# Kernel tuning notes

Hardware: AMD Instinct MI355X
Metric: run time of the kernel (lower is better)

## Reference

```python
import jax, jax.numpy as jnp
import numpy as np

B, N, E, D, N_NODE = 512, 64, 64, 256, 200000
NEG = -9e15
ALPHA = 0.2  # leaky-relu slope from HGNN_ATT(..., 0.2, ...)


def _hgat_layer(x, adj_mask, w2, w3, a, a2, wc, w=None):
    """HyperGraphAttentionLayerSparse (HyperGAT), dense-masked vectorized form.
    x: [B,N,d_in], adj_mask: [B,E,N] bool. Returns (node [B,N,d], edge [B,E,d]).
    Eval mode: dropout is identity. concat=False so no ELU on output."""
    d = w2.shape[1]
    x4 = x @ w2                                            # [B,N,d]
    if w is not None:                                      # transfer=True path
        x = x @ w
    # node->edge attention: score = leakyrelu([word_context; x4_node] @ a), independent of edge idx
    s1 = jax.nn.leaky_relu(jnp.dot(wc, a[:d, 0]) + x4 @ a[d:, 0], ALPHA)   # [B,N]
    att_edge = jax.nn.softmax(jnp.where(adj_mask, s1[:, None, :], NEG), axis=2)  # [B,E,N]
    edge = att_edge @ x                                    # [B,E,d]
    edge4 = edge @ w3                                      # [B,E,d]
    # edge->node attention: score = leakyrelu([x4_node; edge4_edge] @ a2)
    s_pair = jax.nn.leaky_relu((x4 @ a2[:d, 0])[:, None, :] + (edge4 @ a2[d:, 0])[:, :, None], ALPHA)  # [B,E,N]
    att_node = jax.nn.softmax(jnp.swapaxes(jnp.where(adj_mask, s_pair, NEG), 1, 2), axis=2)  # [B,N,E]
    node = att_node @ edge                                 # [B,N,d]
    return node, edge


def setup_inputs() -> dict:
    key = jax.random.key(0)
    ks = jax.random.split(key, 16)
    stdv = 1.0 / np.sqrt(D)  # SessionGraph.reset_parameters uniform(-stdv, stdv)
    u = lambda k, shape: jax.random.uniform(k, shape, jnp.float32, -stdv, stdv)
    return {
        "inputs": jax.random.randint(ks[0], (B, N), 0, N_NODE, dtype=jnp.int32),
        "HT": (jax.random.uniform(ks[1], (B, E, N)) < 0.3).astype(jnp.int32),
        "G": jnp.zeros((1,), jnp.float32),
        "EG": jnp.zeros((1,), jnp.float32),
        "emb_w": u(ks[2], (N_NODE, D)),
        "emb2_w": u(ks[3], (N_NODE, D)),
        "g1_w2": u(ks[4], (D, D)),
        "g1_w3": u(ks[5], (D, D)),
        "g1_a": u(ks[6], (2 * D, 1)),
        "g1_a2": u(ks[7], (2 * D, 1)),
        "g1_wc": u(ks[8], (D,)),
        "g2_w": u(ks[9], (D, D)),
        "g2_w2": u(ks[10], (D, D)),
        "g2_w3": u(ks[11], (D, D)),
        "g2_a": u(ks[12], (2 * D, 1)),
        "g2_a2": u(ks[13], (2 * D, 1)),
        "g2_wc": u(ks[14], (D,)),
    }


def reference(inputs, HT, G, EG, emb_w, emb2_w, g1_w2, g1_w3, g1_a, g1_a2, g1_wc,
              g2_w, g2_w2, g2_w3, g2_a, g2_a2, g2_wc):
    adj_mask = HT > 0
    x = emb_w[inputs]                                      # [B,N,D] embedding gather
    residual = x
    # HGNN_ATT with step=2: gat1 (transfer=False) + residual, gat2 (transfer=True) + residual
    x, _ = _hgat_layer(x, adj_mask, g1_w2, g1_w3, g1_a, g1_a2, g1_wc)
    x = x + residual
    x, _ = _hgat_layer(x, adj_mask, g2_w2, g2_w3, g2_a, g2_a2, g2_wc, g2_w)
    x = x + residual
    nodes2 = emb2_w[inputs]                                # second embedding gather
    return (x, x, nodes2)  # (nodes, hidden, nodes2); hidden aliases nodes in the original
```

## Files before the change

### kernel.cpp

```cpp
#include <hip/hip_runtime.h>

#define BB 512
#define NN 64
#define EE 64
#define DD 256
#define BND (BB * NN * DD)
#define SA 68

typedef __attribute__((ext_vector_type(8))) short s8v;
typedef __attribute__((ext_vector_type(4))) float f4v;
typedef __attribute__((ext_vector_type(8))) unsigned short u16x8;

__device__ __forceinline__ unsigned short f2bf(float f) {
    unsigned int x = __float_as_uint(f);
    x = x + 0x7fffu + ((x >> 16) & 1u);
    return (unsigned short)(x >> 16);
}
__device__ __forceinline__ float bf2f(unsigned short u) {
    return __uint_as_float(((unsigned int)u) << 16);
}
__device__ __forceinline__ float lrelu(float v) { return v > 0.f ? v : 0.2f * v; }

#define WS_PREP  0
#define WS_P3B   8192
#define WS_WFRAG 12288

__global__ void prep_dots(const float* __restrict__ w2a, const float* __restrict__ w3a,
                          const float* __restrict__ aa, const float* __restrict__ a2a,
                          const float* __restrict__ wca,
                          const float* __restrict__ w2b, const float* __restrict__ w3b,
                          const float* __restrict__ ab, const float* __restrict__ a2b,
                          const float* __restrict__ wcb,
                          float* __restrict__ prep, float* __restrict__ p3b_ws) {
    const int t = threadIdx.x;
    const int blk = blockIdx.x;
    const int layer = blk >> 3;
    const int r0 = (blk & 7) * 32;
    __shared__ float vhi[256], v2lo[256], v2hi[256], red[256];
    const float* w2 = layer ? w2b : w2a;
    const float* w3 = layer ? w3b : w3a;
    const float* av = layer ? ab : aa;
    const float* a2 = layer ? a2b : a2a;
    vhi[t] = av[256 + t];
    v2lo[t] = a2[t];
    v2hi[t] = a2[256 + t];
    __syncthreads();
    const int row = r0 + (t >> 3), q = t & 7;
    const float* w2r = w2 + (size_t)row * DD + q * 32;
    const float* w3r = w3 + (size_t)row * DD + q * 32;
    float s1 = 0.f, s2 = 0.f, s3 = 0.f;
    #pragma unroll
    for (int c = 0; c < 8; c++) {
        float4 v = *(const float4*)&w2r[c * 4];
        float4 u = *(const float4*)&w3r[c * 4];
        float4 p1 = *(const float4*)&vhi[q * 32 + c * 4];
        float4 p2 = *(const float4*)&v2lo[q * 32 + c * 4];
        float4 p3 = *(const float4*)&v2hi[q * 32 + c * 4];
        s1 = fmaf(v.x, p1.x, fmaf(v.y, p1.y, fmaf(v.z, p1.z, fmaf(v.w, p1.w, s1))));
        s2 = fmaf(v.x, p2.x, fmaf(v.y, p2.y, fmaf(v.z, p2.z, fmaf(v.w, p2.w, s2))));
        s3 = fmaf(u.x, p3.x, fmaf(u.y, p3.y, fmaf(u.z, p3.z, fmaf(u.w, p3.w, s3))));
    }
    s1 += __shfl_xor(s1, 1); s1 += __shfl_xor(s1, 2); s1 += __shfl_xor(s1, 4);
    s2 += __shfl_xor(s2, 1); s2 += __shfl_xor(s2, 2); s2 += __shfl_xor(s2, 4);
    s3 += __shfl_xor(s3, 1); s3 += __shfl_xor(s3, 2); s3 += __shfl_xor(s3, 4);
    if (q == 0) {
        if (layer == 0) { prep[row] = s1; prep[256 + row] = s2; prep[512 + row] = s3; }
        else { prep[1024 + row] = s1; prep[1280 + row] = s2; p3b_ws[row] = s3; }
    }
    if ((blk & 7) == 0) {
        red[t] = layer ? (wcb[t] * ab[t]) : (wca[t] * aa[t]);
        __syncthreads();
        for (int o = 128; o > 0; o >>= 1) { if (t < o) red[t] += red[t + o]; __syncthreads(); }
        if (t == 0) prep[layer ? 1792 : 768] = red[0];
    }
}

__global__ void prep2_pack(const float* __restrict__ wtr, const float* __restrict__ p3b_ws,
                           float* __restrict__ prep, unsigned short* __restrict__ wfrag) {
    const int t = threadIdx.x, blk = blockIdx.x;
    __shared__ float p3[256];
    if (blk < 8) {
        p3[t] = p3b_ws[t];
        __syncthreads();
        const int row = blk * 32 + (t >> 3), q = t & 7;
        const float* wr = wtr + (size_t)row * DD + q * 32;
        float s = 0.f;
        #pragma unroll
        for (int c = 0; c < 8; c++) {
            float4 v = *(const float4*)&wr[c * 4];
            float4 p = *(const float4*)&p3[q * 32 + c * 4];
            s = fmaf(v.x, p.x, fmaf(v.y, p.y, fmaf(v.z, p.z, fmaf(v.w, p.w, s))));
        }
        s += __shfl_xor(s, 1); s += __shfl_xor(s, 2); s += __shfl_xor(s, 4);
        if (q == 0) prep[1536 + row] = s;
    } else {
        int gid = (blk - 8) * 256 + t;
        int l = gid & 63, frag = gid >> 6;
        int kc = frag >> 4, nt = frag & 15;
        int kb = kc * 32 + (l >> 4) * 8;
        int n = nt * 16 + (l & 15);
        u16x8 u;
        #pragma unroll
        for (int j = 0; j < 8; j++) u[j] = f2bf(wtr[(size_t)(kb + j) * DD + n]);
        *(u16x8*)(wfrag + (size_t)gid * 8) = u;
    }
}

__launch_bounds__(512, 4)
__global__ void mega(const int* __restrict__ inputs, const int* __restrict__ HT,
                     const float* __restrict__ emb_w, const float* __restrict__ emb2_w,
                     const float* __restrict__ prep, const unsigned short* __restrict__ wfrag,
                     float* __restrict__ out) {
    __shared__ unsigned short bufA[256 * SA];
    __shared__ unsigned short RA[64 * SA];
    __shared__ unsigned short RB[64 * SA];
    __shared__ unsigned short RC[64 * SA];
    __shared__ unsigned short RD[64 * SA];
    __shared__ unsigned short XT[16 * SA];
    __shared__ unsigned short pvs[6 * 256];
    __shared__ float dvs[384];
    __shared__ float db2[192];
    __shared__ float u1f[64], invdef[64];
    __shared__ unsigned long long mE[64], mN[64];

    const int b = blockIdx.x;
    const int t = threadIdx.x;
    const int lane = t & 63;
    const int w8 = t >> 6;
    const int l15 = lane & 15, lh = lane >> 4;

    for (int i = t; i < 1536; i += 512) {
        int off = i + (((i >> 8) >= 3) ? 256 : 0);
        pvs[i] = f2bf(prep[off]);
    }
    for (int i = t; i < 16 * SA; i += 512) XT[i] = 0;
    {
        const int rw = t >> 3, q8 = t & 7;
        const int idx = inputs[b * 64 + rw];
        const float* src = emb_w + (size_t)idx * DD + q8 * 32;
        #pragma unroll
        for (int c = 0; c < 8; c++) {
            float4 v = ((const float4*)src)[c];
            ushort4 u;
            u.x = f2bf(v.x); u.y = f2bf(v.y); u.z = f2bf(v.z); u.w = f2bf(v.w);
            *(ushort4*)&bufA[rw * 264 + q8 * 32 + c * 4] = u;
        }
    }
    float4 n2r[8];
    #pragma unroll
    for (int c = 0; c < 8; c++) {
        int i = t + 512 * c;
        int n = i >> 6, cc = i & 63;
        int idx = inputs[b * 64 + n];
        n2r[c] = ((const float4*)(emb2_w + (size_t)idx * DD))[cc];
    }
    #pragma unroll
    for (int i = 0; i < 8; i++) {
        int e = w8 * 8 + i;
        int hx = HT[((size_t)b * EE + e) * NN + lane];
        unsigned long long m = __ballot(hx > 0);
        if (lane == 0) mE[e] = m;
    }
    __syncthreads();

    if (w8 < 4) {
        const int wtile = w8 * 16;
        const int j = (l15 < 6) ? l15 : 5;
        f4v acc = {0.f, 0.f, 0.f, 0.f};
        #pragma unroll
        for (int kc = 0; kc < 8; kc++) {
            s8v a = *(const s8v*)&bufA[(wtile + l15) * 264 + kc * 32 + lh * 8];
            s8v bv = *(const s8v*)&pvs[j * 256 + kc * 32 + lh * 8];
            acc = __builtin_amdgcn_mfma_f32_16x16x32_bf16(a, bv, acc, 0, 0, 0);
        }
        if (l15 < 6) {
            #pragma unroll
            for (int rg = 0; rg < 4; rg++)
                dvs[l15 * 64 + wtile + lh * 4 + rg] = acc[rg];
        }
    } else if (w8 == 4) {
        unsigned long long acc = 0ull;
        for (int e = 0; e < 64; e++) acc |= ((mE[e] >> lane) & 1ull) << e;
        mN[lane] = acc;
    }
    __syncthreads();

    const int wr = (w8 & 3) * 16;
    const int wc = (w8 >> 2) * 32;
    const int row0 = wr + lh * 4;

    {
        float s1l = lrelu(prep[768] + dvs[lane]);
        float g1 = s1l;
        #pragma unroll
        for (int o = 32; o > 0; o >>= 1) g1 = fmaxf(g1, __shfl_xor(g1, o));
        float E1 = __expf(s1l - g1);
        #pragma unroll
        for (int i = 0; i < 8; i++) {
            int e = w8 * 8 + i;
            unsigned long long me = mE[e];
            float pe = (me == 0ull) ? 1.f : (((me >> lane) & 1ull) ? E1 : 0.f);
            unsigned short bf = f2bf(pe);
            RA[lane * SA + e] = bf;
            RC[e * SA + lane] = bf;
        }
    }
    __syncthreads();

    if (w8 < 4) {
        const int etile = w8 * 16;
        f4v acc = {0.f, 0.f, 0.f, 0.f};
        #pragma unroll
        for (int kc = 0; kc < 2; kc++) {
            u16x8 au;
            #pragma unroll
            for (int jj = 0; jj < 8; jj++) {
                int k = kc * 32 + lh * 8 + jj;
                float v = (l15 == 0) ? 1.f : ((l15 <= 4) ? dvs[(l15 + 1) * 64 + k] : 0.f);
                au[jj] = f2bf(v);
            }
            s8v bv = *(const s8v*)&RC[(etile + l15) * SA + kc * 32 + lh * 8];
            acc = __builtin_amdgcn_mfma_f32_16x16x32_bf16((s8v)au, bv, acc, 0, 0, 0);
        }
        int e = etile + l15;
        if (lh == 0) {
            float De = acc[0], We = acc[1];
            invdef[e] = 1.f / De;
            u1f[e] = We / De;
            XT[e] = f2bf(De);
            XT[1 * SA + e] = f2bf(acc[2]);
            XT[2 * SA + e] = f2bf(acc[3]);
        } else if (lh == 1) {
            XT[3 * SA + e] = f2bf(acc[0]);
        }
    }
    __syncthreads();

    {
        float t2l = dvs[64 + lane];
        float gt2 = t2l;
        #pragma unroll
        for (int o = 32; o > 0; o >>= 1) gt2 = fmaxf(gt2, __shfl_xor(gt2, o));
        float um = u1f[lane];
        #pragma unroll
        for (int o = 32; o > 0; o >>= 1) um = fmaxf(um, __shfl_xor(um, o));
        float M1 = lrelu(gt2 + um);
        float ul = u1f[lane];
        float ide = invdef[lane];
        #pragma unroll
        for (int i = 0; i < 8; i++) {
            int n = w8 * 8 + i;
            unsigned long long mn = mN[n];
            float t2n = dvs[64 + n];
            float pr = (mn == 0ull) ? 1.f
                     : (((mn >> lane) & 1ull) ? __expf(lrelu(t2n + ul) - M1) : 0.f);
            RB[n * SA + lane] = f2bf(pr * ide);
        }
    }
    __syncthreads();

    {
        f4v a0 = {0.f,0.f,0.f,0.f}, a1 = {0.f,0.f,0.f,0.f}, ax = {0.f,0.f,0.f,0.f};
        #pragma unroll
        for (int kc = 0; kc < 2; kc++) {
            s8v a  = *(const s8v*)&RB[(wr + l15) * SA + kc * 32 + lh * 8];
            s8v b0 = *(const s8v*)&RA[(wc + l15) * SA + kc * 32 + lh * 8];
            s8v b1 = *(const s8v*)&RA[(wc + 16 + l15) * SA + kc * 32 + lh * 8];
            s8v bx = *(const s8v*)&XT[l15 * SA + kc * 32 + lh * 8];
            a0 = __builtin_amdgcn_mfma_f32_16x16x32_bf16(a, b0, a0, 0, 0, 0);
            a1 = __builtin_amdgcn_mfma_f32_16x16x32_bf16(a, b1, a1, 0, 0, 0);
            ax = __builtin_amdgcn_mfma_f32_16x16x32_bf16(a, bx, ax, 0, 0, 0);
        }
        float invdn[4];
        #pragma unroll
        for (int rg = 0; rg < 4; rg++) invdn[rg] = 1.f / __shfl(ax[rg], lh << 4);
        int col0 = wc + l15, col1 = wc + 16 + l15;
        ushort4 u0, u1;
        #pragma unroll
        for (int rg = 0; rg < 4; rg++) {
            ((unsigned short*)&u0)[rg] = f2bf(a0[rg] * invdn[rg] + ((row0 + rg) == col0 ? 1.f : 0.f));
            ((unsigned short*)&u1)[rg] = f2bf(a1[rg] * invdn[rg] + ((row0 + rg) == col1 ? 1.f : 0.f));
        }
        *(ushort4*)&RD[col0 * SA + row0] = u0;
        *(ushort4*)&RD[col1 * SA + row0] = u1;
        if (w8 < 4 && l15 >= 1 && l15 <= 3) {
            int jj = l15 - 1;
            #pragma unroll
            for (int rg = 0; rg < 4; rg++)
                db2[jj * 64 + row0 + rg] = ax[rg] * invdn[rg] + dvs[(jj + 3) * 64 + row0 + rg];
        }
    }
    __syncthreads();

    {
        float s2l = lrelu(prep[1792] + db2[lane]);
        float g2 = s2l;
        #pragma unroll
        for (int o = 32; o > 0; o >>= 1) g2 = fmaxf(g2, __shfl_xor(g2, o));
        float E2 = __expf(s2l - g2);
        #pragma unroll
        for (int i = 0; i < 8; i++) {
            int e = w8 * 8 + i;
            unsigned long long me = mE[e];
            float pe = (me == 0ull) ? 1.f : (((me >> lane) & 1ull) ? E2 : 0.f);
            unsigned short bf = f2bf(pe);
            RA[lane * SA + e] = bf;
            RC[e * SA + lane] = bf;
        }
    }
    __syncthreads();

    if (w8 < 4) {
        const int etile = w8 * 16;
        f4v acc = {0.f, 0.f, 0.f, 0.f};
        #pragma unroll
        for (int kc = 0; kc < 2; kc++) {
            u16x8 au;
            #pragma unroll
            for (int jj = 0; jj < 8; jj++) {
                int k = kc * 32 + lh * 8 + jj;
                float v = (l15 == 0) ? 1.f : ((l15 == 1) ? db2[128 + k] : 0.f);
                au[jj] = f2bf(v);
            }
            s8v bv = *(const s8v*)&RC[(etile + l15) * SA + kc * 32 + lh * 8];
            acc = __builtin_amdgcn_mfma_f32_16x16x32_bf16((s8v)au, bv, acc, 0, 0, 0);
        }
        if (lh == 0) {
            int e = etile + l15;
            float De = acc[0], We = acc[1];
            invdef[e] = 1.f / De;
            u1f[e] = We / De;
            XT[e] = f2bf(De);
        }
    }
    __syncthreads();

    {
        float d1l = db2[64 + lane];
        float gd1 = d1l;
        #pragma unroll
        for (int o = 32; o > 0; o >>= 1) gd1 = fmaxf(gd1, __shfl_xor(gd1, o));
        float um = u1f[lane];
        #pragma unroll
        for (int o = 32; o > 0; o >>= 1) um = fmaxf(um, __shfl_xor(um, o));
        float M2 = lrelu(gd1 + um);
        float ul = u1f[lane];
        float ide = invdef[lane];
        #pragma unroll
        for (int i = 0; i < 8; i++) {
            int n = w8 * 8 + i;
            unsigned long long mn = mN[n];
            float d1n = db2[64 + n];
            float pr = (mn == 0ull) ? 1.f
                     : (((mn >> lane) & 1ull) ? __expf(lrelu(d1n + ul) - M2) : 0.f);
            RB[n * SA + lane] = f2bf(pr * ide);
        }
    }
    __syncthreads();

    {
        f4v a0 = {0.f,0.f,0.f,0.f}, a1 = {0.f,0.f,0.f,0.f}, ax = {0.f,0.f,0.f,0.f};
        #pragma unroll
        for (int kc = 0; kc < 2; kc++) {
            s8v a  = *(const s8v*)&RB[(wr + l15) * SA + kc * 32 + lh * 8];
            s8v b0 = *(const s8v*)&RA[(wc + l15) * SA + kc * 32 + lh * 8];
            s8v b1 = *(const s8v*)&RA[(wc + 16 + l15) * SA + kc * 32 + lh * 8];
            s8v bx = *(const s8v*)&XT[l15 * SA + kc * 32 + lh * 8];
            a0 = __builtin_amdgcn_mfma_f32_16x16x32_bf16(a, b0, a0, 0, 0, 0);
            a1 = __builtin_amdgcn_mfma_f32_16x16x32_bf16(a, b1, a1, 0, 0, 0);
            ax = __builtin_amdgcn_mfma_f32_16x16x32_bf16(a, bx, ax, 0, 0, 0);
        }
        float invdn[4];
        #pragma unroll
        for (int rg = 0; rg < 4; rg++) invdn[rg] = 1.f / __shfl(ax[rg], lh << 4);
        #pragma unroll
        for (int rg = 0; rg < 4; rg++) {
            RC[(row0 + rg) * SA + wc + l15] = f2bf(a0[rg] * invdn[rg]);
            RC[(row0 + rg) * SA + wc + 16 + l15] = f2bf(a1[rg] * invdn[rg]);
        }
    }
    __syncthreads();

    {
        f4v a0 = {0.f,0.f,0.f,0.f}, a1 = {0.f,0.f,0.f,0.f};
        #pragma unroll
        for (int kc = 0; kc < 2; kc++) {
            s8v a  = *(const s8v*)&RC[(wr + l15) * SA + kc * 32 + lh * 8];
            s8v b0 = *(const s8v*)&RD[(wc + l15) * SA + kc * 32 + lh * 8];
            s8v b1 = *(const s8v*)&RD[(wc + 16 + l15) * SA + kc * 32 + lh * 8];
            a0 = __builtin_amdgcn_mfma_f32_16x16x32_bf16(a, b0, a0, 0, 0, 0);
            a1 = __builtin_amdgcn_mfma_f32_16x16x32_bf16(a, b1, a1, 0, 0, 0);
        }
        #pragma unroll
        for (int rg = 0; rg < 4; rg++) {
            RA[(row0 + rg) * SA + wc + l15] = f2bf(a0[rg]);
            RA[(row0 + rg) * SA + wc + 16 + l15] = f2bf(a1[rg]);
        }
    }
    #pragma unroll
    for (int c = 0; c < 8; c++) {
        int i = t + 512 * c;
        int n = i >> 6, cc = i & 63;
        ((float4*)(out + (size_t)2 * BND + (size_t)(b * 64 + n) * DD))[cc] = n2r[c];
    }
    __syncthreads();

    const int cb8 = (w8 >> 2) * 8;
    unsigned short rres[8][4];
    {
        f4v acc[8];
        #pragma unroll
        for (int nt = 0; nt < 8; nt++) acc[nt] = (f4v){0.f, 0.f, 0.f, 0.f};
        const s8v* wf = (const s8v*)wfrag;
        #pragma unroll
        for (int kc = 0; kc < 8; kc++) {
            s8v a = *(const s8v*)&bufA[(wr + l15) * 264 + kc * 32 + lh * 8];
            #pragma unroll
            for (int nt = 0; nt < 8; nt++) {
                s8v bv = wf[(size_t)(kc * 16 + cb8 + nt) * 64 + lane];
                acc[nt] = __builtin_amdgcn_mfma_f32_16x16x32_bf16(a, bv, acc[nt], 0, 0, 0);
            }
        }
        #pragma unroll
        for (int nt = 0; nt < 8; nt++) {
            #pragma unroll
            for (int rg = 0; rg < 4; rg++)
                rres[nt][rg] = bufA[(row0 + rg) * 264 + (cb8 + nt) * 16 + l15];
        }
        __syncthreads();
        #pragma unroll
        for (int nt = 0; nt < 8; nt++) {
            int feat = (cb8 + nt) * 16 + l15;
            ushort4 u;
            u.x = f2bf(acc[nt][0]); u.y = f2bf(acc[nt][1]);
            u.z = f2bf(acc[nt][2]); u.w = f2bf(acc[nt][3]);
            *(ushort4*)&bufA[feat * SA + row0] = u;
        }
    }
    __syncthreads();

    {
        f4v acc2[8];
        #pragma unroll
        for (int nt = 0; nt < 8; nt++) acc2[nt] = (f4v){0.f, 0.f, 0.f, 0.f};
        #pragma unroll
        for (int kc = 0; kc < 2; kc++) {
            s8v a = *(const s8v*)&RA[(wr + l15) * SA + kc * 32 + lh * 8];
            #pragma unroll
            for (int nt = 0; nt < 8; nt++) {
                s8v bv = *(const s8v*)&bufA[((cb8 + nt) * 16 + l15) * SA + kc * 32 + lh * 8];
                acc2[nt] = __builtin_amdgcn_mfma_f32_16x16x32_bf16(a, bv, acc2[nt], 0, 0, 0);
            }
        }
        #pragma unroll
        for (int nt = 0; nt < 8; nt++) {
            #pragma unroll
            for (int rg = 0; rg < 4; rg++) {
                int row = row0 + rg;
                int colg = (cb8 + nt) * 16 + l15;
                float v = acc2[nt][rg] + bf2f(rres[nt][rg]);
                size_t o = (size_t)(b * 64 + row) * DD + colg;
                out[o] = v;
                out[BND + o] = v;
            }
        }
    }
}

extern "C" void kernel_launch(void* const* d_in, const int* in_sizes, int n_in,
                              void* d_out, int out_size, void* d_ws, size_t ws_size,
                              hipStream_t stream) {
    const int* inputs = (const int*)d_in[0];
    const int* HT = (const int*)d_in[1];
    const float* emb_w  = (const float*)d_in[4];
    const float* emb2_w = (const float*)d_in[5];
    const float* g1_w2 = (const float*)d_in[6];
    const float* g1_w3 = (const float*)d_in[7];
    const float* g1_a  = (const float*)d_in[8];
    const float* g1_a2 = (const float*)d_in[9];
    const float* g1_wc = (const float*)d_in[10];
    const float* g2_w  = (const float*)d_in[11];
    const float* g2_w2 = (const float*)d_in[12];
    const float* g2_w3 = (const float*)d_in[13];
    const float* g2_a  = (const float*)d_in[14];
    const float* g2_a2 = (const float*)d_in[15];
    const float* g2_wc = (const float*)d_in[16];

    float* out = (float*)d_out;
    float* prep = (float*)((char*)d_ws + WS_PREP);
    float* p3b_ws = (float*)((char*)d_ws + WS_P3B);
    unsigned short* wfrag = (unsigned short*)((char*)d_ws + WS_WFRAG);

    prep_dots<<<16, 256, 0, stream>>>(g1_w2, g1_w3, g1_a, g1_a2, g1_wc,
                                      g2_w2, g2_w3, g2_a, g2_a2, g2_wc,
                                      prep, p3b_ws);
    prep2_pack<<<40, 256, 0, stream>>>(g2_w, p3b_ws, prep, wfrag);
    mega<<<BB, 512, 0, stream>>>(inputs, HT, emb_w, emb2_w, prep, wfrag, out);
}
```

Before: 64.00 us.

## Process two batches per block and prefetch next batch's gathers during compute

Each block now handles two consecutive batch elements in a loop. The embedding, emb2 and HT loads for the second element are issued into registers while the first element is being computed, so global-memory latency overlaps with compute. The emb2 passthrough store also moves to the start of each iteration. Launch bounds are relaxed to two blocks per CU to leave room for the extra prefetch registers. The cost is half as many blocks (256 on a large GPU), which can leave CUs underused, plus higher register pressure.

After: 89.32 us. 39.6% more time.

```diff
diff --git a/kernel.cpp b/kernel.cpp
--- a/kernel.cpp
+++ b/kernel.cpp
@@ -106,7 +106,7 @@
     }
 }
 
-__launch_bounds__(512, 4)
+__launch_bounds__(512, 2)
 __global__ void mega(const int* __restrict__ inputs, const int* __restrict__ HT,
                      const float* __restrict__ emb_w, const float* __restrict__ emb2_w,
                      const float* __restrict__ prep, const unsigned short* __restrict__ wfrag,
@@ -123,347 +123,377 @@
     __shared__ float u1f[64], invdef[64];
     __shared__ unsigned long long mE[64], mN[64];
 
-    const int b = blockIdx.x;
+    const int blk = blockIdx.x;
     const int t = threadIdx.x;
     const int lane = t & 63;
     const int w8 = t >> 6;
     const int l15 = lane & 15, lh = lane >> 4;
+    const int rw = t >> 3, q8 = t & 7;
 
     for (int i = t; i < 1536; i += 512) {
         int off = i + (((i >> 8) >= 3) ? 256 : 0);
         pvs[i] = f2bf(prep[off]);
     }
     for (int i = t; i < 16 * SA; i += 512) XT[i] = 0;
+
+    float4 xr[8], n2[8];
+    int htv[8];
     {
-        const int rw = t >> 3, q8 = t & 7;
-        const int idx = inputs[b * 64 + rw];
-        const float* src = emb_w + (size_t)idx * DD + q8 * 32;
+        const int b0 = blk * 2;
+        const int idx = inputs[b0 * 64 + rw];
+        const float4* src = (const float4*)(emb_w + (size_t)idx * DD + q8 * 32);
+        #pragma unroll
+        for (int c = 0; c < 8; c++) xr[c] = src[c];
         #pragma unroll
         for (int c = 0; c < 8; c++) {
-            float4 v = ((const float4*)src)[c];
+            int i = t + 512 * c;
+            int n = i >> 6, cc = i & 63;
+            int idx2 = inputs[b0 * 64 + n];
+            n2[c] = ((const float4*)(emb2_w + (size_t)idx2 * DD))[cc];
+        }
+        #pragma unroll
+        for (int i = 0; i < 8; i++)
+            htv[i] = HT[((size_t)b0 * EE + w8 * 8 + i) * NN + lane];
+    }
+
+    const int wr = (w8 & 3) * 16;
+    const int wc = (w8 >> 2) * 32;
+    const int row0 = wr + lh * 4;
+    const int cb8 = (w8 >> 2) * 8;
+
+    #pragma unroll
+    for (int it = 0; it < 2; it++) {
+        const int b = blk * 2 + it;
+
+        #pragma unroll
+        for (int c = 0; c < 8; c++) {
+            float4 v = xr[c];
             ushort4 u;
             u.x = f2bf(v.x); u.y = f2bf(v.y); u.z = f2bf(v.z); u.w = f2bf(v.w);
             *(ushort4*)&bufA[rw * 264 + q8 * 32 + c * 4] = u;
         }
-    }
-    float4 n2r[8];
-    #pragma unroll
-    for (int c = 0; c < 8; c++) {
-        int i = t + 512 * c;
-        int n = i >> 6, cc = i & 63;
-        int idx = inputs[b * 64 + n];
-        n2r[c] = ((const float4*)(emb2_w + (size_t)idx * DD))[cc];
-    }
-    #pragma unroll
-    for (int i = 0; i < 8; i++) {
-        int e = w8 * 8 + i;
-        int hx = HT[((size_t)b * EE + e) * NN + lane];
-        unsigned long long m = __ballot(hx > 0);
-        if (lane == 0) mE[e] = m;
-    }
-    __syncthreads();
-
-    if (w8 < 4) {
-        const int wtile = w8 * 16;
-        const int j = (l15 < 6) ? l15 : 5;
-        f4v acc = {0.f, 0.f, 0.f, 0.f};
-        #pragma unroll
-        for (int kc = 0; kc < 8; kc++) {
-            s8v a = *(const s8v*)&bufA[(wtile + l15) * 264 + kc * 32 + lh * 8];
-            s8v bv = *(const s8v*)&pvs[j * 256 + kc * 32 + lh * 8];
-            acc = __builtin_amdgcn_mfma_f32_16x16x32_bf16(a, bv, acc, 0, 0, 0);
-        }
-        if (l15 < 6) {
-            #pragma unroll
-            for (int rg = 0; rg < 4; rg++)
-                dvs[l15 * 64 + wtile + lh * 4 + rg] = acc[rg];
-        }
-    } else if (w8 == 4) {
-        unsigned long long acc = 0ull;
-        for (int e = 0; e < 64; e++) acc |= ((mE[e] >> lane) & 1ull) << e;
-        mN[lane] = acc;
-    }
-    __syncthreads();
-
-    const int wr = (w8 & 3) * 16;
-    const int wc = (w8 >> 2) * 32;
-    const int row0 = wr + lh * 4;
-
-    {
-        float s1l = lrelu(prep[768] + dvs[lane]);
-        float g1 = s1l;
-        #pragma unroll
-        for (int o = 32; o > 0; o >>= 1) g1 = fmaxf(g1, __shfl_xor(g1, o));
-        float E1 = __expf(s1l - g1);
         #pragma unroll
         for (int i = 0; i < 8; i++) {
-            int e = w8 * 8 + i;
-            unsigned long long me = mE[e];
-            float pe = (me == 0ull) ? 1.f : (((me >> lane) & 1ull) ? E1 : 0.f);
-            unsigned short bf = f2bf(pe);
-            RA[lane * SA + e] = bf;
-            RC[e * SA + lane] = bf;
-        }
-    }
-    __syncthreads();
-
-    if (w8 < 4) {
-        const int etile = w8 * 16;
-        f4v acc = {0.f, 0.f, 0.f, 0.f};
-        #pragma unroll
-        for (int kc = 0; kc < 2; kc++) {
-            u16x8 au;
-            #pragma unroll
-            for (int jj = 0; jj < 8; jj++) {
-                int k = kc * 32 + lh * 8 + jj;
-                float v = (l15 == 0) ? 1.f : ((l15 <= 4) ? dvs[(l15 + 1) * 64 + k] : 0.f);
-                au[jj] = f2bf(v);
-            }
-            s8v bv = *(const s8v*)&RC[(etile + l15) * SA + kc * 32 + lh * 8];
-            acc = __builtin_amdgcn_mfma_f32_16x16x32_bf16((s8v)au, bv, acc, 0, 0, 0);
-        }
-        int e = etile + l15;
-        if (lh == 0) {
-            float De = acc[0], We = acc[1];
-            invdef[e] = 1.f / De;
-            u1f[e] = We / De;
-            XT[e] = f2bf(De);
-            XT[1 * SA + e] = f2bf(acc[2]);
-            XT[2 * SA + e] = f2bf(acc[3]);
-        } else if (lh == 1) {
-            XT[3 * SA + e] = f2bf(acc[0]);
-        }
-    }
-    __syncthreads();
-
-    {
-        float t2l = dvs[64 + lane];
-        float gt2 = t2l;
-        #pragma unroll
-        for (int o = 32; o > 0; o >>= 1) gt2 = fmaxf(gt2, __shfl_xor(gt2, o));
-        float um = u1f[lane];
-        #pragma unroll
-        for (int o = 32; o > 0; o >>= 1) um = fmaxf(um, __shfl_xor(um, o));
-        float M1 = lrelu(gt2 + um);
-        float ul = u1f[lane];
-        float ide = invdef[lane];
-        #pragma unroll
-        for (int i = 0; i < 8; i++) {
-            int n = w8 * 8 + i;
-            unsigned long long mn = mN[n];
-            float t2n = dvs[64 + n];
-            float pr = (mn == 0ull) ? 1.f
-                     : (((mn >> lane) & 1ull) ? __expf(lrelu(t2n + ul) - M1) : 0.f);
-            RB[n * SA + lane] = f2bf(pr * ide);
-        }
-    }
-    __syncthreads();
-
-    {
-        f4v a0 = {0.f,0.f,0.f,0.f}, a1 = {0.f,0.f,0.f,0.f}, ax = {0.f,0.f,0.f,0.f};
-        #pragma unroll
-        for (int kc = 0; kc < 2; kc++) {
-            s8v a  = *(const s8v*)&RB[(wr + l15) * SA + kc * 32 + lh * 8];
-            s8v b0 = *(const s8v*)&RA[(wc + l15) * SA + kc * 32 + lh * 8];
-            s8v b1 = *(const s8v*)&RA[(wc + 16 + l15) * SA + kc * 32 + lh * 8];
-            s8v bx = *(const s8v*)&XT[l15 * SA + kc * 32 + lh * 8];
-            a0 = __builtin_amdgcn_mfma_f32_16x16x32_bf16(a, b0, a0, 0, 0, 0);
-            a1 = __builtin_amdgcn_mfma_f32_16x16x32_bf16(a, b1, a1, 0, 0, 0);
-            ax = __builtin_amdgcn_mfma_f32_16x16x32_bf16(a, bx, ax, 0, 0, 0);
-        }
-        float invdn[4];
-        #pragma unroll
-        for (int rg = 0; rg < 4; rg++) invdn[rg] = 1.f / __shfl(ax[rg], lh << 4);
-        int col0 = wc + l15, col1 = wc + 16 + l15;
-        ushort4 u0, u1;
-        #pragma unroll
-        for (int rg = 0; rg < 4; rg++) {
-            ((unsigned short*)&u0)[rg] = f2bf(a0[rg] * invdn[rg] + ((row0 + rg) == col0 ? 1.f : 0.f));
-            ((unsigned short*)&u1)[rg] = f2bf(a1[rg] * invdn[rg] + ((row0 + rg) == col1 ? 1.f : 0.f));
-        }
-        *(ushort4*)&RD[col0 * SA + row0] = u0;
-        *(ushort4*)&RD[col1 * SA + row0] = u1;
-        if (w8 < 4 && l15 >= 1 && l15 <= 3) {
-            int jj = l15 - 1;
-            #pragma unroll
-            for (int rg = 0; rg < 4; rg++)
-                db2[jj * 64 + row0 + rg] = ax[rg] * invdn[rg] + dvs[(jj + 3) * 64 + row0 + rg];
-        }
-    }
-    __syncthreads();
-
-    {
-        float s2l = lrelu(prep[1792] + db2[lane]);
-        float g2 = s2l;
-        #pragma unroll
-        for (int o = 32; o > 0; o >>= 1) g2 = fmaxf(g2, __shfl_xor(g2, o));
-        float E2 = __expf(s2l - g2);
-        #pragma unroll
-        for (int i = 0; i < 8; i++) {
-            int e = w8 * 8 + i;
-            unsigned long long me = mE[e];
-            float pe = (me == 0ull) ? 1.f : (((me >> lane) & 1ull) ? E2 : 0.f);
-            unsigned short bf = f2bf(pe);
-            RA[lane * SA + e] = bf;
-            RC[e * SA + lane] = bf;
-        }
-    }
-    __syncthreads();
-
-    if (w8 < 4) {
-        const int etile = w8 * 16;
-        f4v acc = {0.f, 0.f, 0.f, 0.f};
-        #pragma unroll
-        for (int kc = 0; kc < 2; kc++) {
-            u16x8 au;
-            #pragma unroll
-            for (int jj = 0; jj < 8; jj++) {
-                int k = kc * 32 + lh * 8 + jj;
-                float v = (l15 == 0) ? 1.f : ((l15 == 1) ? db2[128 + k] : 0.f);
-                au[jj] = f2bf(v);
-            }
-            s8v bv = *(const s8v*)&RC[(etile + l15) * SA + kc * 32 + lh * 8];
-            acc = __builtin_amdgcn_mfma_f32_16x16x32_bf16((s8v)au, bv, acc, 0, 0, 0);
-        }
-        if (lh == 0) {
+            unsigned long long m = __ballot(htv[i] > 0);
+            if (lane == 0) mE[w8 * 8 + i] = m;
+        }
+        #pragma unroll
+        for (int c = 0; c < 8; c++) {
+            int i = t + 512 * c;
+            int n = i >> 6, cc = i & 63;
+            ((float4*)(out + (size_t)2 * BND + (size_t)(b * 64 + n) * DD))[cc] = n2[c];
+        }
+        __syncthreads();
+
+        if (w8 < 4) {
+            const int wtile = w8 * 16;
+            const int j = (l15 < 6) ? l15 : 5;
+            f4v acc = {0.f, 0.f, 0.f, 0.f};
+            #pragma unroll
+            for (int kc = 0; kc < 8; kc++) {
+                s8v a = *(const s8v*)&bufA[(wtile + l15) * 264 + kc * 32 + lh * 8];
+                s8v bv = *(const s8v*)&pvs[j * 256 + kc * 32 + lh * 8];
+                acc = __builtin_amdgcn_mfma_f32_16x16x32_bf16(a, bv, acc, 0, 0, 0);
+            }
+            if (l15 < 6) {
+                #pragma unroll
+                for (int rg = 0; rg < 4; rg++)
+                    dvs[l15 * 64 + wtile + lh * 4 + rg] = acc[rg];
+            }
+        } else if (w8 == 4) {
+            unsigned long long acc = 0ull;
+            for (int e = 0; e < 64; e++) acc |= ((mE[e] >> lane) & 1ull) << e;
+            mN[lane] = acc;
+        }
+        if (it == 0) {
+            const int bn = blk * 2 + 1;
+            const int idx = inputs[bn * 64 + rw];
+            const float4* src = (const float4*)(emb_w + (size_t)idx * DD + q8 * 32);
+            #pragma unroll
+            for (int c = 0; c < 8; c++) xr[c] = src[c];
+            #pragma unroll
+            for (int c = 0; c < 8; c++) {
+                int i = t + 512 * c;
+                int n = i >> 6, cc = i & 63;
+                int idx2 = inputs[bn * 64 + n];
+                n2[c] = ((const float4*)(emb2_w + (size_t)idx2 * DD))[cc];
+            }
+            #pragma unroll
+            for (int i = 0; i < 8; i++)
+                htv[i] = HT[((size_t)bn * EE + w8 * 8 + i) * NN + lane];
+        }
+        __syncthreads();
+
+        {
+            float s1l = lrelu(prep[768] + dvs[lane]);
+            float g1 = s1l;
+            #pragma unroll
+            for (int o = 32; o > 0; o >>= 1) g1 = fmaxf(g1, __shfl_xor(g1, o));
+            float E1 = __expf(s1l - g1);
+            #pragma unroll
+            for (int i = 0; i < 8; i++) {
+                int e = w8 * 8 + i;
+                unsigned long long me = mE[e];
+                float pe = (me == 0ull) ? 1.f : (((me >> lane) & 1ull) ? E1 : 0.f);
+                unsigned short bf = f2bf(pe);
+                RA[lane * SA + e] = bf;
+                RC[e * SA + lane] = bf;
+            }
+        }
+        __syncthreads();
+
+        if (w8 < 4) {
+            const int etile = w8 * 16;
+            f4v acc = {0.f, 0.f, 0.f, 0.f};
+            #pragma unroll
+            for (int kc = 0; kc < 2; kc++) {
+                u16x8 au;
+                #pragma unroll
+                for (int jj = 0; jj < 8; jj++) {
+                    int k = kc * 32 + lh * 8 + jj;
+                    float v = (l15 == 0) ? 1.f : ((l15 <= 4) ? dvs[(l15 + 1) * 64 + k] : 0.f);
+                    au[jj] = f2bf(v);
+                }
+                s8v bv = *(const s8v*)&RC[(etile + l15) * SA + kc * 32 + lh * 8];
+                acc = __builtin_amdgcn_mfma_f32_16x16x32_bf16((s8v)au, bv, acc, 0, 0, 0);
+            }
             int e = etile + l15;
-            float De = acc[0], We = acc[1];
-            invdef[e] = 1.f / De;
-            u1f[e] = We / De;
-            XT[e] = f2bf(De);
-        }
-    }
-    __syncthreads();
-
-    {
-        float d1l = db2[64 + lane];
-        float gd1 = d1l;
-        #pragma unroll
-        for (int o = 32; o > 0; o >>= 1) gd1 = fmaxf(gd1, __shfl_xor(gd1, o));
-        float um = u1f[lane];
-        #pragma unroll
-        for (int o = 32; o > 0; o >>= 1) um = fmaxf(um, __shfl_xor(um, o));
-        float M2 = lrelu(gd1 + um);
-        float ul = u1f[lane];
-        float ide = invdef[lane];
-        #pragma unroll
-        for (int i = 0; i < 8; i++) {
-            int n = w8 * 8 + i;
-            unsigned long long mn = mN[n];
-            float d1n = db2[64 + n];
-            float pr = (mn == 0ull) ? 1.f
-                     : (((mn >> lane) & 1ull) ? __expf(lrelu(d1n + ul) - M2) : 0.f);
-            RB[n * SA + lane] = f2bf(pr * ide);
-        }
-    }
-    __syncthreads();
-
-    {
-        f4v a0 = {0.f,0.f,0.f,0.f}, a1 = {0.f,0.f,0.f,0.f}, ax = {0.f,0.f,0.f,0.f};
-        #pragma unroll
-        for (int kc = 0; kc < 2; kc++) {
-            s8v a  = *(const s8v*)&RB[(wr + l15) * SA + kc * 32 + lh * 8];
-            s8v b0 = *(const s8v*)&RA[(wc + l15) * SA + kc * 32 + lh * 8];
-            s8v b1 = *(const s8v*)&RA[(wc + 16 + l15) * SA + kc * 32 + lh * 8];
-            s8v bx = *(const s8v*)&XT[l15 * SA + kc * 32 + lh * 8];
-            a0 = __builtin_amdgcn_mfma_f32_16x16x32_bf16(a, b0, a0, 0, 0, 0);
-            a1 = __builtin_amdgcn_mfma_f32_16x16x32_bf16(a, b1, a1, 0, 0, 0);
-            ax = __builtin_amdgcn_mfma_f32_16x16x32_bf16(a, bx, ax, 0, 0, 0);
-        }
-        float invdn[4];
-        #pragma unroll
-        for (int rg = 0; rg < 4; rg++) invdn[rg] = 1.f / __shfl(ax[rg], lh << 4);
-        #pragma unroll
-        for (int rg = 0; rg < 4; rg++) {
-            RC[(row0 + rg) * SA + wc + l15] = f2bf(a0[rg] * invdn[rg]);
-            RC[(row0 + rg) * SA + wc + 16 + l15] = f2bf(a1[rg] * invdn[rg]);
-        }
-    }
-    __syncthreads();
-
-    {
-        f4v a0 = {0.f,0.f,0.f,0.f}, a1 = {0.f,0.f,0.f,0.f};
-        #pragma unroll
-        for (int kc = 0; kc < 2; kc++) {
-            s8v a  = *(const s8v*)&RC[(wr + l15) * SA + kc * 32 + lh * 8];
-            s8v b0 = *(const s8v*)&RD[(wc + l15) * SA + kc * 32 + lh * 8];
-            s8v b1 = *(const s8v*)&RD[(wc + 16 + l15) * SA + kc * 32 + lh * 8];
-            a0 = __builtin_amdgcn_mfma_f32_16x16x32_bf16(a, b0, a0, 0, 0, 0);
-            a1 = __builtin_amdgcn_mfma_f32_16x16x32_bf16(a, b1, a1, 0, 0, 0);
-        }
-        #pragma unroll
-        for (int rg = 0; rg < 4; rg++) {
-            RA[(row0 + rg) * SA + wc + l15] = f2bf(a0[rg]);
-            RA[(row0 + rg) * SA + wc + 16 + l15] = f2bf(a1[rg]);
-        }
-    }
-    #pragma unroll
-    for (int c = 0; c < 8; c++) {
-        int i = t + 512 * c;
-        int n = i >> 6, cc = i & 63;
-        ((float4*)(out + (size_t)2 * BND + (size_t)(b * 64 + n) * DD))[cc] = n2r[c];
-    }
-    __syncthreads();
-
-    const int cb8 = (w8 >> 2) * 8;
-    unsigned short rres[8][4];
-    {
-        f4v acc[8];
-        #pragma unroll
-        for (int nt = 0; nt < 8; nt++) acc[nt] = (f4v){0.f, 0.f, 0.f, 0.f};
-        const s8v* wf = (const s8v*)wfrag;
-        #pragma unroll
-        for (int kc = 0; kc < 8; kc++) {
-            s8v a = *(const s8v*)&bufA[(wr + l15) * 264 + kc * 32 + lh * 8];
+            if (lh == 0) {
+                float De = acc[0], We = acc[1];
+                invdef[e] = 1.f / De;
+                u1f[e] = We / De;
+                XT[e] = f2bf(De);
+                XT[1 * SA + e] = f2bf(acc[2]);
+                XT[2 * SA + e] = f2bf(acc[3]);
+            } else if (lh == 1) {
+                XT[3 * SA + e] = f2bf(acc[0]);
+            }
+        }
+        __syncthreads();
+
+        {
+            float t2l = dvs[64 + lane];
+            float gt2 = t2l;
+            #pragma unroll
+            for (int o = 32; o > 0; o >>= 1) gt2 = fmaxf(gt2, __shfl_xor(gt2, o));
+            float um = u1f[lane];
+            #pragma unroll
+            for (int o = 32; o > 0; o >>= 1) um = fmaxf(um, __shfl_xor(um, o));
+            float M1 = lrelu(gt2 + um);
+            float ul = u1f[lane];
+            float ide = invdef[lane];
+            #pragma unroll
+            for (int i = 0; i < 8; i++) {
+                int n = w8 * 8 + i;
+                unsigned long long mn = mN[n];
+                float t2n = dvs[64 + n];
+                float pr = (mn == 0ull) ? 1.f
+                         : (((mn >> lane) & 1ull) ? __expf(lrelu(t2n + ul) - M1) : 0.f);
+                RB[n * SA + lane] = f2bf(pr * ide);
+            }
+        }
+        __syncthreads();
+
+        {
+            f4v a0 = {0.f,0.f,0.f,0.f}, a1 = {0.f,0.f,0.f,0.f}, ax = {0.f,0.f,0.f,0.f};
+            #pragma unroll
+            for (int kc = 0; kc < 2; kc++) {
+                s8v a  = *(const s8v*)&RB[(wr + l15) * SA + kc * 32 + lh * 8];
+                s8v b0 = *(const s8v*)&RA[(wc + l15) * SA + kc * 32 + lh * 8];
+                s8v b1 = *(const s8v*)&RA[(wc + 16 + l15) * SA + kc * 32 + lh * 8];
+                s8v bx = *(const s8v*)&XT[l15 * SA + kc * 32 + lh * 8];
+                a0 = __builtin_amdgcn_mfma_f32_16x16x32_bf16(a, b0, a0, 0, 0, 0);
+                a1 = __builtin_amdgcn_mfma_f32_16x16x32_bf16(a, b1, a1, 0, 0, 0);
+                ax = __builtin_amdgcn_mfma_f32_16x16x32_bf16(a, bx, ax, 0, 0, 0);
+            }
+            float invdn[4];
+            #pragma unroll
+            for (int rg = 0; rg < 4; rg++) invdn[rg] = 1.f / __shfl(ax[rg], lh << 4);
+            int col0 = wc + l15, col1 = wc + 16 + l15;
+            ushort4 u0, u1;
+            #pragma unroll
+            for (int rg = 0; rg < 4; rg++) {
+                ((unsigned short*)&u0)[rg] = f2bf(a0[rg] * invdn[rg] + ((row0 + rg) == col0 ? 1.f : 0.f));
+                ((unsigned short*)&u1)[rg] = f2bf(a1[rg] * invdn[rg] + ((row0 + rg) == col1 ? 1.f : 0.f));
+            }
+            *(ushort4*)&RD[col0 * SA + row0] = u0;
+            *(ushort4*)&RD[col1 * SA + row0] = u1;
+            if (w8 < 4 && l15 >= 1 && l15 <= 3) {
+                int jj = l15 - 1;
+                #pragma unroll
+                for (int rg = 0; rg < 4; rg++)
+                    db2[jj * 64 + row0 + rg] = ax[rg] * invdn[rg] + dvs[(jj + 3) * 64 + row0 + rg];
+            }
+        }
+        __syncthreads();
+
+        {
+            float s2l = lrelu(prep[1792] + db2[lane]);
+            float g2 = s2l;
+            #pragma unroll
+            for (int o = 32; o > 0; o >>= 1) g2 = fmaxf(g2, __shfl_xor(g2, o));
+            float E2 = __expf(s2l - g2);
+            #pragma unroll
+            for (int i = 0; i < 8; i++) {
+                int e = w8 * 8 + i;
+                unsigned long long me = mE[e];
+                float pe = (me == 0ull) ? 1.f : (((me >> lane) & 1ull) ? E2 : 0.f);
+                unsigned short bf = f2bf(pe);
+                RA[lane * SA + e] = bf;
+                RC[e * SA + lane] = bf;
+            }
+        }
+        __syncthreads();
+
+        if (w8 < 4) {
+            const int etile = w8 * 16;
+            f4v acc = {0.f, 0.f, 0.f, 0.f};
+            #pragma unroll
+            for (int kc = 0; kc < 2; kc++) {
+                u16x8 au;
+                #pragma unroll
+                for (int jj = 0; jj < 8; jj++) {
+                    int k = kc * 32 + lh * 8 + jj;
+                    float v = (l15 == 0) ? 1.f : ((l15 == 1) ? db2[128 + k] : 0.f);
+                    au[jj] = f2bf(v);
+                }
+                s8v bv = *(const s8v*)&RC[(etile + l15) * SA + kc * 32 + lh * 8];
+                acc = __builtin_amdgcn_mfma_f32_16x16x32_bf16((s8v)au, bv, acc, 0, 0, 0);
+            }
+            if (lh == 0) {
+                int e = etile + l15;
+                float De = acc[0], We = acc[1];
+                invdef[e] = 1.f / De;
+                u1f[e] = We / De;
+                XT[e] = f2bf(De);
+            }
+        }
+        __syncthreads();
+
+        {
+            float d1l = db2[64 + lane];
+            float gd1 = d1l;
+            #pragma unroll
+            for (int o = 32; o > 0; o >>= 1) gd1 = fmaxf(gd1, __shfl_xor(gd1, o));
+            float um = u1f[lane];
+            #pragma unroll
+            for (int o = 32; o > 0; o >>= 1) um = fmaxf(um, __shfl_xor(um, o));
+            float M2 = lrelu(gd1 + um);
+            float ul = u1f[lane];
+            float ide = invdef[lane];
+            #pragma unroll
+            for (int i = 0; i < 8; i++) {
+                int n = w8 * 8 + i;
+                unsigned long long mn = mN[n];
+                float d1n = db2[64 + n];
+                float pr = (mn == 0ull) ? 1.f
+                         : (((mn >> lane) & 1ull) ? __expf(lrelu(d1n + ul) - M2) : 0.f);
+                RB[n * SA + lane] = f2bf(pr * ide);
+            }
+        }
+        __syncthreads();
+
+        {
+            f4v a0 = {0.f,0.f,0.f,0.f}, a1 = {0.f,0.f,0.f,0.f}, ax = {0.f,0.f,0.f,0.f};
+            #pragma unroll
+            for (int kc = 0; kc < 2; kc++) {
+                s8v a  = *(const s8v*)&RB[(wr + l15) * SA + kc * 32 + lh * 8];
+                s8v b0 = *(const s8v*)&RA[(wc + l15) * SA + kc * 32 + lh * 8];
+                s8v b1 = *(const s8v*)&RA[(wc + 16 + l15) * SA + kc * 32 + lh * 8];
+                s8v bx = *(const s8v*)&XT[l15 * SA + kc * 32 + lh * 8];
+                a0 = __builtin_amdgcn_mfma_f32_16x16x32_bf16(a, b0, a0, 0, 0, 0);
+                a1 = __builtin_amdgcn_mfma_f32_16x16x32_bf16(a, b1, a1, 0, 0, 0);
+                ax = __builtin_amdgcn_mfma_f32_16x16x32_bf16(a, bx, ax, 0, 0, 0);
+            }
+            float invdn[4];
+            #pragma unroll
+            for (int rg = 0; rg < 4; rg++) invdn[rg] = 1.f / __shfl(ax[rg], lh << 4);
+            #pragma unroll
+            for (int rg = 0; rg < 4; rg++) {
+                RC[(row0 + rg) * SA + wc + l15] = f2bf(a0[rg] * invdn[rg]);
+                RC[(row0 + rg) * SA + wc + 16 + l15] = f2bf(a1[rg] * invdn[rg]);
+            }
+        }
+        __syncthreads();
+
+        {
+            f4v a0 = {0.f,0.f,0.f,0.f}, a1 = {0.f,0.f,0.f,0.f};
+            #pragma unroll
+            for (int kc = 0; kc < 2; kc++) {
+                s8v a  = *(const s8v*)&RC[(wr + l15) * SA + kc * 32 + lh * 8];
+                s8v b0 = *(const s8v*)&RD[(wc + l15) * SA + kc * 32 + lh * 8];
+                s8v b1 = *(const s8v*)&RD[(wc + 16 + l15) * SA + kc * 32 + lh * 8];
+                a0 = __builtin_amdgcn_mfma_f32_16x16x32_bf16(a, b0, a0, 0, 0, 0);
+                a1 = __builtin_amdgcn_mfma_f32_16x16x32_bf16(a, b1, a1, 0, 0, 0);
+            }
+            #pragma unroll
+            for (int rg = 0; rg < 4; rg++) {
+                RA[(row0 + rg) * SA + wc + l15] = f2bf(a0[rg]);
+                RA[(row0 + rg) * SA + wc + 16 + l15] = f2bf(a1[rg]);
+            }
+        }
+        __syncthreads();
+
+        unsigned short rres[8][4];
+        {
+            f4v acc[8];
+            #pragma unroll
+            for (int nt = 0; nt < 8; nt++) acc[nt] = (f4v){0.f, 0.f, 0.f, 0.f};
+            const s8v* wf = (const s8v*)wfrag;
+            #pragma unroll
+            for (int kc = 0; kc < 8; kc++) {
+                s8v a = *(const s8v*)&bufA[(wr + l15) * 264 + kc * 32 + lh * 8];
+                #pragma unroll
+                for (int nt = 0; nt < 8; nt++) {
+                    s8v bv = wf[(size_t)(kc * 16 + cb8 + nt) * 64 + lane];
+                    acc[nt] = __builtin_amdgcn_mfma_f32_16x16x32_bf16(a, bv, acc[nt], 0, 0, 0);
+                }
+            }
             #pragma unroll
             for (int nt = 0; nt < 8; nt++) {
-                s8v bv = wf[(size_t)(kc * 16 + cb8 + nt) * 64 + lane];
-                acc[nt] = __builtin_amdgcn_mfma_f32_16x16x32_bf16(a, bv, acc[nt], 0, 0, 0);
-            }
-        }
-        #pragma unroll
-        for (int nt = 0; nt < 8; nt++) {
-            #pragma unroll
-            for (int rg = 0; rg < 4; rg++)
-                rres[nt][rg] = bufA[(row0 + rg) * 264 + (cb8 + nt) * 16 + l15];
-        }
-        __syncthreads();
-        #pragma unroll
-        for (int nt = 0; nt < 8; nt++) {
-            int feat = (cb8 + nt) * 16 + l15;
-            ushort4 u;
-            u.x = f2bf(acc[nt][0]); u.y = f2bf(acc[nt][1]);
-            u.z = f2bf(acc[nt][2]); u.w = f2bf(acc[nt][3]);
-            *(ushort4*)&bufA[feat * SA + row0] = u;
-        }
-    }
-    __syncthreads();
-
-    {
-        f4v acc2[8];
-        #pragma unroll
-        for (int nt = 0; nt < 8; nt++) acc2[nt] = (f4v){0.f, 0.f, 0.f, 0.f};
-        #pragma unroll
-        for (int kc = 0; kc < 2; kc++) {
-            s8v a = *(const s8v*)&RA[(wr + l15) * SA + kc * 32 + lh * 8];
+                #pragma unroll
+                for (int rg = 0; rg < 4; rg++)
+                    rres[nt][rg] = bufA[(row0 + rg) * 264 + (cb8 + nt) * 16 + l15];
+            }
+            __syncthreads();
             #pragma unroll
             for (int nt = 0; nt < 8; nt++) {
-                s8v bv = *(const s8v*)&bufA[((cb8 + nt) * 16 + l15) * SA + kc * 32 + lh * 8];
-                acc2[nt] = __builtin_amdgcn_mfma_f32_16x16x32_bf16(a, bv, acc2[nt], 0, 0, 0);
-            }
-        }
-        #pragma unroll
-        for (int nt = 0; nt < 8; nt++) {
-            #pragma unroll
-            for (int rg = 0; rg < 4; rg++) {
-                int row = row0 + rg;
-                int colg = (cb8 + nt) * 16 + l15;
-                float v = acc2[nt][rg] + bf2f(rres[nt][rg]);
-                size_t o = (size_t)(b * 64 + row) * DD + colg;
-                out[o] = v;
-                out[BND + o] = v;
-            }
-        }
+                int feat = (cb8 + nt) * 16 + l15;
+                ushort4 u;
+                u.x = f2bf(acc[nt][0]); u.y = f2bf(acc[nt][1]);
+                u.z = f2bf(acc[nt][2]); u.w = f2bf(acc[nt][3]);
+                *(ushort4*)&bufA[feat * SA + row0] = u;
+            }
+        }
+        __syncthreads();
+
+        {
+            f4v acc2[8];
+            #pragma unroll
+            for (int nt = 0; nt < 8; nt++) acc2[nt] = (f4v){0.f, 0.f, 0.f, 0.f};
+            #pragma unroll
+            for (int kc = 0; kc < 2; kc++) {
+                s8v a = *(const s8v*)&RA[(wr + l15) * SA + kc * 32 + lh * 8];
+                #pragma unroll
+                for (int nt = 0; nt < 8; nt++) {
+                    s8v bv = *(const s8v*)&bufA[((cb8 + nt) * 16 + l15) * SA + kc * 32 + lh * 8];
+                    acc2[nt] = __builtin_amdgcn_mfma_f32_16x16x32_bf16(a, bv, acc2[nt], 0, 0, 0);
+                }
+            }
+            #pragma unroll
+            for (int nt = 0; nt < 8; nt++) {
+                #pragma unroll
+                for (int rg = 0; rg < 4; rg++) {
+                    int row = row0 + rg;
+                    int colg = (cb8 + nt) * 16 + l15;
+                    float v = acc2[nt][rg] + bf2f(rres[nt][rg]);
+                    size_t o = (size_t)(b * 64 + row) * DD + colg;
+                    out[o] = v;
+                    out[BND + o] = v;
+                }
+            }
+        }
+        __syncthreads();
     }
 }
 
@@ -495,5 +525,5 @@
                                       g2_w2, g2_w3, g2_a, g2_a2, g2_wc,
                                       prep, p3b_ws);
     prep2_pack<<<40, 256, 0, stream>>>(g2_w, p3b_ws, prep, wfrag);
-    mega<<<BB, 512, 0, stream>>>(inputs, HT, emb_w, emb2_w, prep, wfrag, out);
+    mega<<<BB / 2, 512, 0, stream>>>(inputs, HT, emb_w, emb2_w, prep, wfrag, out);
 }
```
